# Kernel tuning notes

Measured on AMD Instinct MI355X. Metric: run time of the kernel, lower is better.

## Reference

```python
import jax, jax.numpy as jnp
import numpy as np

B, T, E, H, D = 256, 256, 384, 6, 64  # batch, seq (<= block_size 256), n_embed, n_head, head_size


def setup_inputs() -> dict:
    key = jax.random.key(0)
    ks = jax.random.split(key, 6)
    s = 0.02
    return {
        "x": jax.random.normal(ks[0], (B, T, E), dtype=jnp.float32),
        "Wq": jax.random.normal(ks[1], (H, E, D), dtype=jnp.float32) * s,
        "Wk": jax.random.normal(ks[2], (H, E, D), dtype=jnp.float32) * s,
        "Wv": jax.random.normal(ks[3], (H, E, D), dtype=jnp.float32) * s,
        "Wo": jax.random.normal(ks[4], (E, E), dtype=jnp.float32) * s,
        "bo": jnp.zeros((E,), dtype=jnp.float32),
    }


def reference(x, Wq, Wk, Wv, Wo, bo):
    # per-head projections (bias-free Linears), batched over heads
    q = jnp.einsum("bse,hed->bhsd", x, Wq)
    k = jnp.einsum("bse,hed->bhsd", x, Wk)
    v = jnp.einsum("bse,hed->bhsd", x, Wv)
    scale = jnp.asarray(D, x.dtype) ** -0.5
    scores = jnp.einsum("bhsd,bhtd->bhst", q, k) * scale  # [B,H,T,T]
    causal = jnp.tril(jnp.ones((T, T), dtype=bool))
    scores = jnp.where(causal, scores, jnp.asarray(-jnp.inf, x.dtype))
    attn = jax.nn.softmax(scores, axis=-1)  # dropout = identity (eval)
    out = jnp.einsum("bhst,bhtd->bhsd", attn, v)
    out = out.transpose(0, 2, 1, 3).reshape(B, T, H * D)  # concat heads
    return out @ Wo + bo  # output projection; dropout = identity (eval)
```

## Files before the change

kernel.cpp:

```cpp
#include <hip/hip_runtime.h>
#include <hip/hip_bf16.h>
#include <math.h>

#define BB 256
#define TT 256
#define EE 384
#define HH 6
#define DD 64

typedef __attribute__((ext_vector_type(8))) short bf16x8;
typedef __attribute__((ext_vector_type(4))) float f32x4;

__device__ inline unsigned short f2bf(float f) {
  unsigned int u = __builtin_bit_cast(unsigned int, f);
  u += 0x7fffu + ((u >> 16) & 1u);
  return (unsigned short)(u >> 16);
}

__device__ __forceinline__ void g2l16(const unsigned short* g, unsigned short* l) {
  __builtin_amdgcn_global_load_lds(
      (const __attribute__((address_space(1))) void*)g,
      (__attribute__((address_space(3))) void*)l, 16, 0, 0);
}

#define CVT_BLOCKS 24576
__global__ __launch_bounds__(256) void prep_kernel(const float* __restrict__ x,
                                                   const float* __restrict__ Wq,
                                                   const float* __restrict__ Wk,
                                                   const float* __restrict__ Wv,
                                                   const float* __restrict__ Wo,
                                                   unsigned short* __restrict__ xb,
                                                   unsigned short* __restrict__ Wt) {
  int bid = blockIdx.x;
  if (bid < CVT_BLOCKS) {
    int i = bid * 256 + threadIdx.x;
    float4 f = ((const float4*)x)[i];
    ushort4 o;
    o.x = f2bf(f.x); o.y = f2bf(f.y); o.z = f2bf(f.z); o.w = f2bf(f.w);
    ((ushort4*)xb)[i] = o;
  } else {
    int idx = (bid - CVT_BLOCKS) * 256 + threadIdx.x;
    int n = idx / 384, k = idx % 384;
    float val;
    if (n < 1152) {
      int mat = n / 384;
      int c = n % 384;
      int h = c >> 6, d = c & 63;
      const float* W = (mat == 0) ? Wq : (mat == 1 ? Wk : Wv);
      val = W[((size_t)h * EE + k) * DD + d];
    } else {
      int c = n - 1152;
      val = Wo[(size_t)k * EE + c];
    }
    Wt[idx] = f2bf(val);
  }
}

#define STAGE_T(buf, k0, Bsrc)                                                  \
  do {                                                                          \
    unsigned short* As_ = (unsigned short*)(smem + (buf) * 32768);              \
    unsigned short* Bs_ = As_ + 8192;                                           \
    _Pragma("unroll") for (int i = 0; i < 4; ++i) {                             \
      int rl = rl_base + i * 8;                                                 \
      int gcb = sb ^ (rl & 7);                                                  \
      g2l16(A + (size_t)(m0 + rl) * EE + (k0) + gcb * 8,                        \
            &As_[(wave * 32 + i * 8) * 64]);                                    \
    }                                                                           \
    _Pragma("unroll") for (int i = 0; i < 4; ++i) {                             \
      int rl = rl_base + i * 8;                                                 \
      int gcb = sb ^ (rl & 7);                                                  \
      g2l16((Bsrc) + (size_t)(n0 + rl) * EE + (k0) + gcb * 8,                   \
            &Bs_[(wave * 32 + i * 8) * 64]);                                    \
    }                                                                           \
  } while (0)

#define COMPUTE_T(buf)                                                          \
  do {                                                                          \
    const unsigned short* As_ = (const unsigned short*)(smem + (buf) * 32768);  \
    const unsigned short* Bs_ = As_ + 8192;                                     \
    _Pragma("unroll") for (int kc = 0; kc < 2; ++kc) {                          \
      bf16x8 af[4], bfr[4];                                                     \
      _Pragma("unroll") for (int mi = 0; mi < 4; ++mi)                          \
          af[mi] = *(const bf16x8*)&As_[(wm + mi * 16 + l15) * 64 +             \
                                        ((kc * 4 + quad) ^ xs) * 8];            \
      _Pragma("unroll") for (int ni = 0; ni < 4; ++ni)                          \
          bfr[ni] = *(const bf16x8*)&Bs_[(wn + ni * 16 + l15) * 64 +            \
                                         ((kc * 4 + quad) ^ xs) * 8];           \
      _Pragma("unroll") for (int mi = 0; mi < 4; ++mi)                          \
          _Pragma("unroll") for (int ni = 0; ni < 4; ++ni)                      \
              acc[mi][ni] = __builtin_amdgcn_mfma_f32_16x16x32_bf16(            \
                  af[mi], bfr[ni], acc[mi][ni], 0, 0, 0);                       \
    }                                                                           \
  } while (0)

__global__ __launch_bounds__(256, 2) void qkv128_kernel(const unsigned short* __restrict__ A,
                                                        const unsigned short* __restrict__ Wt,
                                                        unsigned short* __restrict__ q,
                                                        unsigned short* __restrict__ k,
                                                        unsigned short* __restrict__ v) {
  const int L = blockIdx.x;
  const int xcd = L & 7;
  const int j = L >> 3;
  const int mt = xcd * 64 + j / 9;
  const int bx = j % 9;
  const int m0 = mt * 128;
  const int n0 = bx * 128;

  __shared__ char smem[65536];
  unsigned short* bounce = (unsigned short*)smem;

  const int tid = threadIdx.x;
  const int wave = tid >> 6, lane = tid & 63;
  const int l15 = lane & 15, quad = lane >> 4;
  const int wm = (wave & 1) * 64, wn = (wave >> 1) * 64;
  const int xs = l15 & 7;

  f32x4 acc[4][4];
#pragma unroll
  for (int i = 0; i < 4; ++i)
#pragma unroll
    for (int jj = 0; jj < 4; ++jj) acc[i][jj] = (f32x4){0.f, 0.f, 0.f, 0.f};

  const int rl_base = wave * 32 + (lane >> 3);
  const int sb = lane & 7;

  STAGE_T(0, 0, Wt);
  __syncthreads();
#pragma unroll
  for (int it = 0; it < 6; ++it) {
    if (it < 5) STAGE_T((it & 1) ^ 1, (it + 1) * 64, Wt);
    COMPUTE_T(it & 1);
    __syncthreads();
  }

  const int b = m0 >> 8;
  const int t0 = m0 & 255;

  if (bx < 6) {
    unsigned short* outp = (bx < 3) ? q : k;
    const float qs = (bx < 3) ? 0.125f : 1.0f;
    const int cmbase = n0 - (bx < 3 ? 0 : 384);
#pragma unroll
    for (int ni = 0; ni < 4; ++ni) {
      int c = cmbase + wn + ni * 16 + l15;
      int h = c >> 6, d = c & 63;
#pragma unroll
      for (int mi = 0; mi < 4; ++mi)
#pragma unroll
        for (int r = 0; r < 4; ++r) {
          int t = t0 + wm + mi * 16 + quad * 4 + r;
          outp[(((size_t)b * HH + h) * TT + t) * DD + d] = f2bf(acc[mi][ni][r] * qs);
        }
    }
  } else {
#pragma unroll
    for (int pass = 0; pass < 2; ++pass) {
      __syncthreads();
      if ((wave >> 1) == pass) {
#pragma unroll
        for (int ni = 0; ni < 4; ++ni) {
          int cl = ni * 16 + l15;
#pragma unroll
          for (int mi = 0; mi < 4; ++mi)
#pragma unroll
            for (int r = 0; r < 4; ++r) {
              int rloc = wm + mi * 16 + quad * 4 + r;
              bounce[cl * 136 + rloc] = f2bf(acc[mi][ni][r]);
            }
        }
      }
      __syncthreads();
      int h = (bx - 6) * 2 + pass;
      int d = tid >> 2;
      int tb = (tid & 3) * 32;
      unsigned short* vdst = v + (((size_t)b * HH + h) * DD + d) * TT + t0 + tb;
      const unsigned short* bsrc = &bounce[d * 136 + tb];
#pragma unroll
      for (int jj = 0; jj < 4; ++jj)
        *(uint4*)(vdst + jj * 8) = *(const uint4*)(bsrc + jj * 8);
    }
  }
}

__global__ __launch_bounds__(256) void attn_kernel(const unsigned short* __restrict__ q,
                                                   const unsigned short* __restrict__ k,
                                                   const unsigned short* __restrict__ v,
                                                   unsigned short* __restrict__ att) {
  const int L = blockIdx.x;
  const int xcd = L & 7;
  const int j = L >> 3;
  const int bh = xcd * 192 + (j >> 2);
  const int q0 = (j & 3) * 64;
  const int b = bh / HH, h = bh % HH;

  __shared__ unsigned short Ks[64 * 72];
  __shared__ unsigned short Vt[64 * 72];
  __shared__ unsigned short Ps[64 * 72];

  const int tid = threadIdx.x;
  const int wave = tid >> 6, lane = tid & 63;
  const int l15 = lane & 15, quad = lane >> 4;
  const int koff = quad * 8;

  const int sr = tid >> 2, sc = (tid & 3) * 16;
  const unsigned short* kbase = k + ((size_t)bh * TT + sr) * DD + sc;
  const unsigned short* vbase = v + ((size_t)bh * DD + sr) * TT + sc;

  bf16x8 aq[2];
  {
    const unsigned short* qrow =
        q + ((size_t)bh * TT + q0 + wave * 16 + l15) * DD + koff;
    aq[0] = *(const bf16x8*)(qrow);
    aq[1] = *(const bf16x8*)(qrow + 32);
  }

  uint4 kr0 = *(const uint4*)(kbase);
  uint4 kr1 = *(const uint4*)(kbase + 8);
  uint4 vr0 = *(const uint4*)(vbase);
  uint4 vr1 = *(const uint4*)(vbase + 8);
  *(uint4*)&Ks[sr * 72 + sc]     = kr0;
  *(uint4*)&Ks[sr * 72 + sc + 8] = kr1;
  *(uint4*)&Vt[sr * 72 + sc]     = vr0;
  *(uint4*)&Vt[sr * 72 + sc + 8] = vr1;
  __syncthreads();

  f32x4 o_acc[4] = {{0.f,0.f,0.f,0.f},{0.f,0.f,0.f,0.f},{0.f,0.f,0.f,0.f},{0.f,0.f,0.f,0.f}};
  float m_run[4] = {-INFINITY, -INFINITY, -INFINITY, -INFINITY};
  float l_run[4] = {0.f, 0.f, 0.f, 0.f};

  for (int j0 = 0; j0 <= q0; j0 += 64) {
    const bool has_next = (j0 + 64 <= q0);
    if (has_next) {
      const unsigned short* kn = kbase + (size_t)(j0 + 64) * DD;
      const unsigned short* vn = vbase + (j0 + 64);
      kr0 = *(const uint4*)(kn);
      kr1 = *(const uint4*)(kn + 8);
      vr0 = *(const uint4*)(vn);
      vr1 = *(const uint4*)(vn + 8);
    }

    f32x4 s_acc[4] = {{0.f,0.f,0.f,0.f},{0.f,0.f,0.f,0.f},{0.f,0.f,0.f,0.f},{0.f,0.f,0.f,0.f}};
    __builtin_amdgcn_s_setprio(1);
#pragma unroll
    for (int kc = 0; kc < 2; ++kc) {
#pragma unroll
      for (int ct = 0; ct < 4; ++ct) {
        bf16x8 bb = *(const bf16x8*)&Ks[(ct * 16 + l15) * 72 + kc * 32 + koff];
        s_acc[ct] = __builtin_amdgcn_mfma_f32_16x16x32_bf16(aq[kc], bb, s_acc[ct], 0, 0, 0);
      }
    }
    __builtin_amdgcn_s_setprio(0);

    const bool diag = (j0 == q0);
    const int rowbase = q0 + wave * 16 + quad * 4;
#pragma unroll
    for (int r = 0; r < 4; ++r) {
      int qrow = rowbase + r;
      float sv[4];
#pragma unroll
      for (int ct = 0; ct < 4; ++ct) {
        float s = s_acc[ct][r];
        if (diag && (j0 + ct * 16 + l15) > qrow) s = -INFINITY;
        sv[ct] = s;
      }
      float mt = fmaxf(fmaxf(sv[0], sv[1]), fmaxf(sv[2], sv[3]));
      mt = fmaxf(mt, __shfl_xor(mt, 1));
      mt = fmaxf(mt, __shfl_xor(mt, 2));
      mt = fmaxf(mt, __shfl_xor(mt, 4));
      mt = fmaxf(mt, __shfl_xor(mt, 8));
      float mnew = fmaxf(m_run[r], mt);
      float alpha = __expf(m_run[r] - mnew);
      float psum = 0.f;
      int prow = (wave * 16 + quad * 4 + r) * 72;
#pragma unroll
      for (int ct = 0; ct < 4; ++ct) {
        float p = __expf(sv[ct] - mnew);
        psum += p;
        Ps[prow + ct * 16 + l15] = f2bf(p);
      }
      psum += __shfl_xor(psum, 1);
      psum += __shfl_xor(psum, 2);
      psum += __shfl_xor(psum, 4);
      psum += __shfl_xor(psum, 8);
      l_run[r] = l_run[r] * alpha + psum;
      m_run[r] = mnew;
#pragma unroll
      for (int dt = 0; dt < 4; ++dt) o_acc[dt][r] *= alpha;
    }

    __builtin_amdgcn_s_setprio(1);
#pragma unroll
    for (int kc = 0; kc < 2; ++kc) {
      bf16x8 a = *(const bf16x8*)&Ps[(wave * 16 + l15) * 72 + kc * 32 + koff];
#pragma unroll
      for (int dt = 0; dt < 4; ++dt) {
        bf16x8 bb = *(const bf16x8*)&Vt[(dt * 16 + l15) * 72 + kc * 32 + koff];
        o_acc[dt] = __builtin_amdgcn_mfma_f32_16x16x32_bf16(a, bb, o_acc[dt], 0, 0, 0);
      }
    }
    __builtin_amdgcn_s_setprio(0);

    if (has_next) {
      __syncthreads();
      *(uint4*)&Ks[sr * 72 + sc]     = kr0;
      *(uint4*)&Ks[sr * 72 + sc + 8] = kr1;
      *(uint4*)&Vt[sr * 72 + sc]     = vr0;
      *(uint4*)&Vt[sr * 72 + sc + 8] = vr1;
      __syncthreads();
    }
  }

#pragma unroll
  for (int dt = 0; dt < 4; ++dt) {
#pragma unroll
    for (int r = 0; r < 4; ++r) {
      int row = wave * 16 + quad * 4 + r;
      int t = q0 + row;
      int d = dt * 16 + l15;
      float o = o_acc[dt][r] / l_run[r];
      att[(((size_t)b * TT + t) * HH + h) * DD + d] = f2bf(o);
    }
  }
}

__global__ __launch_bounds__(256, 2) void oproj128_kernel(const unsigned short* __restrict__ A,
                                                          const unsigned short* __restrict__ Wot,
                                                          const float* __restrict__ bo,
                                                          float* __restrict__ out) {
  const int L = blockIdx.x;
  const int xcd = L & 7;
  const int j = L >> 3;
  const int mt = xcd * 64 + j / 3;
  const int bx = j % 3;
  const int m0 = mt * 128;
  const int n0 = bx * 128;

  __shared__ char smem[65536];

  const int tid = threadIdx.x;
  const int wave = tid >> 6, lane = tid & 63;
  const int l15 = lane & 15, quad = lane >> 4;
  const int wm = (wave & 1) * 64, wn = (wave >> 1) * 64;
  const int xs = l15 & 7;

  f32x4 acc[4][4];
#pragma unroll
  for (int i = 0; i < 4; ++i)
#pragma unroll
    for (int jj = 0; jj < 4; ++jj) acc[i][jj] = (f32x4){0.f, 0.f, 0.f, 0.f};

  const int rl_base = wave * 32 + (lane >> 3);
  const int sb = lane & 7;

  STAGE_T(0, 0, Wot);
  __syncthreads();
#pragma unroll
  for (int it = 0; it < 6; ++it) {
    if (it < 5) STAGE_T((it & 1) ^ 1, (it + 1) * 64, Wot);
    COMPUTE_T(it & 1);
    __syncthreads();
  }

#pragma unroll
  for (int ni = 0; ni < 4; ++ni) {
    int c = n0 + wn + ni * 16 + l15;
    float bias = bo[c];
#pragma unroll
    for (int mi = 0; mi < 4; ++mi)
#pragma unroll
      for (int r = 0; r < 4; ++r) {
        int m = m0 + wm + mi * 16 + quad * 4 + r;
        out[(size_t)m * EE + c] = acc[mi][ni][r] + bias;
      }
  }
}

extern "C" void kernel_launch(void* const* d_in, const int* in_sizes, int n_in,
                              void* d_out, int out_size, void* d_ws, size_t ws_size,
                              hipStream_t stream) {
  const float* x  = (const float*)d_in[0];
  const float* Wq = (const float*)d_in[1];
  const float* Wk = (const float*)d_in[2];
  const float* Wv = (const float*)d_in[3];
  const float* Wo = (const float*)d_in[4];
  const float* bo = (const float*)d_in[5];
  float* out = (float*)d_out;

  char* ws = (char*)d_ws;
  const size_t SZ = (size_t)BB * TT * EE * 2;
  const size_t SQ = (size_t)BB * HH * TT * DD * 2;
  unsigned short* xb = (unsigned short*)ws;
  unsigned short* q  = (unsigned short*)(ws + SZ);
  unsigned short* k  = (unsigned short*)(ws + SZ + SQ);
  unsigned short* v  = (unsigned short*)(ws + SZ + 2 * SQ);
  unsigned short* Wt = (unsigned short*)(ws + SZ + 3 * SQ);
  unsigned short* att = xb;

  prep_kernel<<<CVT_BLOCKS + 2304, 256, 0, stream>>>(x, Wq, Wk, Wv, Wo, xb, Wt);
  qkv128_kernel<<<dim3(9 * (BB * TT) / 128), 256, 0, stream>>>(xb, Wt, q, k, v);
  attn_kernel<<<dim3(BB * HH * TT / 64), 256, 0, stream>>>(q, k, v, att);
  oproj128_kernel<<<dim3(3 * (BB * TT) / 128), 256, 0, stream>>>(att, Wt + 1152 * 384, bo, out);
}
```

Measured before the change: 376.1 us.

## Load K and V MFMA fragments directly from global memory, dropping LDS staging

The attention kernel no longer stages K and V tiles through shared memory with register prefetch and block barriers. Each wave now loads its MFMA B-operand fragments for K and V straight from global memory every iteration. This removes the LDS writes, LDS reads and two __syncthreads per tile and cuts LDS use. In exchange, every one of the four waves loads the same K/V data separately, so global and L2 traffic rises. The loads are also no longer prefetched one tile ahead, which exposes more memory latency.

```diff
diff --git a/kernel.cpp b/kernel.cpp
--- a/kernel.cpp
+++ b/kernel.cpp
@@ -193,18 +193,12 @@
   const int q0 = (j & 3) * 64;
   const int b = bh / HH, h = bh % HH;
 
-  __shared__ unsigned short Ks[64 * 72];
-  __shared__ unsigned short Vt[64 * 72];
   __shared__ unsigned short Ps[64 * 72];
 
   const int tid = threadIdx.x;
   const int wave = tid >> 6, lane = tid & 63;
   const int l15 = lane & 15, quad = lane >> 4;
   const int koff = quad * 8;
-
-  const int sr = tid >> 2, sc = (tid & 3) * 16;
-  const unsigned short* kbase = k + ((size_t)bh * TT + sr) * DD + sc;
-  const unsigned short* vbase = v + ((size_t)bh * DD + sr) * TT + sc;
 
   bf16x8 aq[2];
   {
@@ -214,42 +208,39 @@
     aq[1] = *(const bf16x8*)(qrow + 32);
   }
 
-  uint4 kr0 = *(const uint4*)(kbase);
-  uint4 kr1 = *(const uint4*)(kbase + 8);
-  uint4 vr0 = *(const uint4*)(vbase);
-  uint4 vr1 = *(const uint4*)(vbase + 8);
-  *(uint4*)&Ks[sr * 72 + sc]     = kr0;
-  *(uint4*)&Ks[sr * 72 + sc + 8] = kr1;
-  *(uint4*)&Vt[sr * 72 + sc]     = vr0;
-  *(uint4*)&Vt[sr * 72 + sc + 8] = vr1;
-  __syncthreads();
+  const unsigned short* kfb = k + ((size_t)bh * TT + l15) * DD + koff;
+  const unsigned short* vfb = v + ((size_t)bh * DD + l15) * TT + koff;
 
   f32x4 o_acc[4] = {{0.f,0.f,0.f,0.f},{0.f,0.f,0.f,0.f},{0.f,0.f,0.f,0.f},{0.f,0.f,0.f,0.f}};
   float m_run[4] = {-INFINITY, -INFINITY, -INFINITY, -INFINITY};
   float l_run[4] = {0.f, 0.f, 0.f, 0.f};
 
   for (int j0 = 0; j0 <= q0; j0 += 64) {
-    const bool has_next = (j0 + 64 <= q0);
-    if (has_next) {
-      const unsigned short* kn = kbase + (size_t)(j0 + 64) * DD;
-      const unsigned short* vn = vbase + (j0 + 64);
-      kr0 = *(const uint4*)(kn);
-      kr1 = *(const uint4*)(kn + 8);
-      vr0 = *(const uint4*)(vn);
-      vr1 = *(const uint4*)(vn + 8);
-    }
+    bf16x8 kb[8];
+#pragma unroll
+    for (int kc = 0; kc < 2; ++kc)
+#pragma unroll
+      for (int ct = 0; ct < 4; ++ct)
+        kb[kc * 4 + ct] =
+            *(const bf16x8*)(kfb + (size_t)(j0 + ct * 16) * DD + kc * 32);
 
     f32x4 s_acc[4] = {{0.f,0.f,0.f,0.f},{0.f,0.f,0.f,0.f},{0.f,0.f,0.f,0.f},{0.f,0.f,0.f,0.f}};
     __builtin_amdgcn_s_setprio(1);
 #pragma unroll
-    for (int kc = 0; kc < 2; ++kc) {
-#pragma unroll
-      for (int ct = 0; ct < 4; ++ct) {
-        bf16x8 bb = *(const bf16x8*)&Ks[(ct * 16 + l15) * 72 + kc * 32 + koff];
-        s_acc[ct] = __builtin_amdgcn_mfma_f32_16x16x32_bf16(aq[kc], bb, s_acc[ct], 0, 0, 0);
-      }
-    }
+    for (int kc = 0; kc < 2; ++kc)
+#pragma unroll
+      for (int ct = 0; ct < 4; ++ct)
+        s_acc[ct] = __builtin_amdgcn_mfma_f32_16x16x32_bf16(aq[kc], kb[kc * 4 + ct],
+                                                            s_acc[ct], 0, 0, 0);
     __builtin_amdgcn_s_setprio(0);
+
+    bf16x8 vb[8];
+#pragma unroll
+    for (int kc = 0; kc < 2; ++kc)
+#pragma unroll
+      for (int dt = 0; dt < 4; ++dt)
+        vb[kc * 4 + dt] =
+            *(const bf16x8*)(vfb + (size_t)(dt * 16) * TT + j0 + kc * 32);
 
     const bool diag = (j0 == q0);
     const int rowbase = q0 + wave * 16 + quad * 4;
@@ -293,21 +284,11 @@
     for (int kc = 0; kc < 2; ++kc) {
       bf16x8 a = *(const bf16x8*)&Ps[(wave * 16 + l15) * 72 + kc * 32 + koff];
 #pragma unroll
-      for (int dt = 0; dt < 4; ++dt) {
-        bf16x8 bb = *(const bf16x8*)&Vt[(dt * 16 + l15) * 72 + kc * 32 + koff];
-        o_acc[dt] = __builtin_amdgcn_mfma_f32_16x16x32_bf16(a, bb, o_acc[dt], 0, 0, 0);
-      }
+      for (int dt = 0; dt < 4; ++dt)
+        o_acc[dt] = __builtin_amdgcn_mfma_f32_16x16x32_bf16(a, vb[kc * 4 + dt],
+                                                            o_acc[dt], 0, 0, 0);
     }
     __builtin_amdgcn_s_setprio(0);
-
-    if (has_next) {
-      __syncthreads();
-      *(uint4*)&Ks[sr * 72 + sc]     = kr0;
-      *(uint4*)&Ks[sr * 72 + sc + 8] = kr1;
-      *(uint4*)&Vt[sr * 72 + sc]     = vr0;
-      *(uint4*)&Vt[sr * 72 + sc + 8] = vr1;
-      __syncthreads();
-    }
   }
 
 #pragma unroll
```

Measured after the change: 471.5 us. 1.25x slower.
